# Kernel optimization log

Measured on AMD Instinct MI355X. Metric: run time of the kernel, lower is better.

## Reference

```python
import jax, jax.numpy as jnp
import numpy as np

B, T, IN, H = 512, 2048, 2, 128


def setup_inputs() -> dict:
    key = jax.random.key(0)
    ks = jax.random.split(key, 14)
    u = lambda k, shape: jax.random.uniform(k, shape, jnp.float32, -0.1, 0.1)
    return {
        "x": jax.random.normal(ks[0], (B, T, IN), jnp.float32),
        "mask": jnp.ones((B, T), jnp.float32),
        "emb_W": u(ks[1], (H, IN)), "emb_b": u(ks[2], (H,)),
        "enc_W": u(ks[3], (H, H)), "enc_b": u(ks[4], (H,)),
        "dec_input": u(ks[5], (H,)), "Vec": u(ks[6], (H,)),
        "Wq_W": u(ks[7], (H, H)), "Wq_b": u(ks[8], (H,)),
        "Wref_W": u(ks[9], (H, H)), "Wref_b": u(ks[10], (H,)),
        "fc1_W": u(ks[11], (H, H)), "fc2_W": u(ks[12], (2, H)),
    }


def reference(x, mask, emb_W, emb_b, enc_W, enc_b, dec_input, Vec,
              Wq_W, Wq_b, Wref_W, Wref_b, fc1_W, fc2_W):
    # Embedding: (B,T,IN) -> (B,T,H)
    x_embed = jnp.einsum("bti,hi->bth", x, emb_W) + emb_b
    # Encoder (stand-in for external Encoder class): per-token Linear + mask
    ref = (jnp.einsum("bti,hi->bth", x_embed, enc_W) + enc_b) * mask[:, :, None]

    def glimpse(query, ref):
        # query: (B,H); ref: (B,T,H)
        u1 = query @ Wq_W.T + Wq_b                                  # (B,H)
        # Conv1d kernel size 1 == pointwise linear over hidden dim
        u2 = jnp.einsum("bti,oi->bot", ref, Wref_W) + Wref_b[None, :, None]  # (B,H,T)
        u = jnp.einsum("h,bht->bt", Vec, jnp.tanh(u1[:, :, None] + u2))      # (B,T)
        a = jax.nn.softmax(u, axis=1)                               # (B,T)
        return jnp.einsum("bht,bt->bh", u2, a)                      # (B,H)

    query = jnp.broadcast_to(dec_input, (x.shape[0], dec_input.shape[0]))
    for _ in range(2):
        query = glimpse(query, ref)

    # final2FC: Linear(no bias) -> ReLU -> Linear(no bias); squeeze(-1) twice is a no-op (last dim=2)
    pred_l = jax.nn.relu(query @ fc1_W.T) @ fc2_W.T                 # (B,2)
    return pred_l
```

## Files before the change

### kernel.cpp

```cpp
#include <hip/hip_runtime.h>
#include <hip/hip_bf16.h>


#define Bsz 512
#define Tsz 2048
#define Hsz 128
#define THR 256
#define TOK 2
#define QB 4
static_assert(QB * THR * TOK == Tsz, "token tiling must cover each row exactly");

#define C2LOG2E 2.8853900817779268f
#define LOG2E   1.4426950408889634f

__device__ __forceinline__ float exp2fast(float x) { return __builtin_amdgcn_exp2f(x); }
__device__ __forceinline__ float rcpfast(float x)  { return __builtin_amdgcn_rcpf(x); }

__global__ __launch_bounds__(128) void kprep(
        const float* __restrict__ embW, const float* __restrict__ embB,
        const float* __restrict__ encW, const float* __restrict__ encB,
        const float* __restrict__ wrefW, const float* __restrict__ wrefB,
        const float* __restrict__ wqW, const float* __restrict__ wqB,
        const float* __restrict__ dec, const float* __restrict__ vec,
        float4* __restrict__ SCA, float4* __restrict__ UC, float* __restrict__ V2G) {
    __shared__ float m0[Hsz], m1[Hsz], cc[Hsz], dq[Hsz];
    int h = threadIdx.x;
    float a0 = 0.f, a1 = 0.f, ac = 0.f;
    for (int k = 0; k < Hsz; ++k) {
        float w = encW[h * Hsz + k];
        a0 = fmaf(w, embW[2 * k + 0], a0);
        a1 = fmaf(w, embW[2 * k + 1], a1);
        ac = fmaf(w, embB[k], ac);
    }
    m0[h] = a0; m1[h] = a1; cc[h] = ac + encB[h]; dq[h] = dec[h];
    __syncthreads();
    float p0 = 0.f, p1 = 0.f, pe = 0.f, uq = wqB[h];
    for (int k = 0; k < Hsz; ++k) {
        float w = wrefW[h * Hsz + k];
        p0 = fmaf(w, m0[k], p0);
        p1 = fmaf(w, m1[k], p1);
        pe = fmaf(w, cc[k], pe);
        uq = fmaf(wqW[h * Hsz + k], dq[k], uq);
    }
    float wb = wrefB[h];
    SCA[h] = make_float4(C2LOG2E * p0, C2LOG2E * p1, C2LOG2E * pe, C2LOG2E * (uq + wb));
    UC[h]  = make_float4(p0, p1, pe, wb);
    V2G[h] = 2.f * vec[h];
}

__global__ __launch_bounds__(THR) void kscore(
        const float* __restrict__ x, const float* __restrict__ mask,
        const float4* __restrict__ quadG, int bstride,
        const float* __restrict__ V2G,
        float4* __restrict__ statsOut) {
    __shared__ float4 quad[Hsz];
    __shared__ float v2s[Hsz];
    __shared__ float4 wr4[THR / 64];
    int blk = blockIdx.x, tid = threadIdx.x;
    int b = blk >> 2, qb = blk & 3;
    int wave = tid >> 6, lane = tid & 63;
    if (tid < Hsz) {
        quad[tid] = quadG[(size_t)b * bstride + tid];
        v2s[tid] = V2G[tid];
    }

    size_t tok0 = (size_t)b * Tsz + (size_t)qb * (THR * TOK);
    const float2* x2 = (const float2*)(x + tok0 * 2);
    const float* mrow = mask + tok0;
    float xm0[TOK], xm1[TOK], mk[TOK];
    #pragma unroll
    for (int j = 0; j < TOK; ++j) {
        float2 xv = x2[j * THR + tid];
        float m = mrow[j * THR + tid];
        mk[j] = m; xm0[j] = xv.x * m; xm1[j] = xv.y * m;
    }
    __syncthreads();

    float acc[TOK] = {0.f, 0.f};
    #pragma unroll 8
    for (int h = 0; h < Hsz; ++h) {
        float4 qd = quad[h];
        float vv = v2s[h];
        #pragma unroll
        for (int j = 0; j < TOK; ++j) {
            float a = fmaf(xm0[j], qd.x, fmaf(xm1[j], qd.y, fmaf(mk[j], qd.z, qd.w)));
            acc[j] = fmaf(vv, rcpfast(exp2fast(a) + 1.f), acc[j]);
        }
    }

    float Z = 0.f, Sm = 0.f, S0 = 0.f, S1 = 0.f;
    #pragma unroll
    for (int j = 0; j < TOK; ++j) {
        float e = exp2fast(-LOG2E * acc[j]);
        Z += e;
        Sm = fmaf(e, mk[j], Sm);
        S0 = fmaf(e, xm0[j], S0);
        S1 = fmaf(e, xm1[j], S1);
    }
    for (int off = 32; off; off >>= 1) {
        Z += __shfl_xor(Z, off); Sm += __shfl_xor(Sm, off);
        S0 += __shfl_xor(S0, off); S1 += __shfl_xor(S1, off);
    }
    if (lane == 0) wr4[wave] = make_float4(Z, Sm, S0, S1);
    __syncthreads();
    if (tid == 0) {
        float4 s = wr4[0];
        #pragma unroll
        for (int w = 1; w < THR / 64; ++w) {
            s.x += wr4[w].x; s.y += wr4[w].y; s.z += wr4[w].z; s.w += wr4[w].w;
        }
        statsOut[blk] = s;
    }
}

__global__ __launch_bounds__(128) void kmid(
        const float4* __restrict__ statsA, const float4* __restrict__ UC,
        const float4* __restrict__ SCA,
        const float* __restrict__ wqW, const float* __restrict__ wqB,
        float4* __restrict__ QB1) {
    __shared__ float q[Hsz];
    int b = blockIdx.x, tid = threadIdx.x;
    float Z = 0.f, Sm = 0.f, S0 = 0.f, S1 = 0.f;
    #pragma unroll
    for (int i = 0; i < QB; ++i) {
        float4 t = statsA[b * QB + i];
        Z += t.x; Sm += t.y; S0 += t.z; S1 += t.w;
    }
    float inv = 1.f / Z;
    float X0 = S0 * inv, X1 = S1 * inv, Cm = Sm * inv;
    float4 u4 = UC[tid];
    q[tid] = fmaf(X0, u4.x, fmaf(X1, u4.y, fmaf(Cm, u4.z, u4.w)));
    __syncthreads();
    float s = wqB[tid];
    const float* wr = wqW + (size_t)tid * Hsz;
    #pragma unroll 8
    for (int k = 0; k < Hsz; ++k) s = fmaf(wr[k], q[k], s);
    float4 sc = SCA[tid];
    QB1[b * Hsz + tid] = make_float4(sc.x, sc.y, sc.z, C2LOG2E * (s + u4.w));
}

__global__ __launch_bounds__(128) void kfin(
        const float4* __restrict__ statsB, const float4* __restrict__ UC,
        const float* __restrict__ fc1, const float* __restrict__ fc2,
        float* __restrict__ out) {
    __shared__ float q[Hsz], rr[Hsz];
    int b = blockIdx.x, tid = threadIdx.x;
    float Z = 0.f, Sm = 0.f, S0 = 0.f, S1 = 0.f;
    #pragma unroll
    for (int i = 0; i < QB; ++i) {
        float4 t = statsB[b * QB + i];
        Z += t.x; Sm += t.y; S0 += t.z; S1 += t.w;
    }
    float inv = 1.f / Z;
    float X0 = S0 * inv, X1 = S1 * inv, Cm = Sm * inv;
    float4 u4 = UC[tid];
    q[tid] = fmaf(X0, u4.x, fmaf(X1, u4.y, fmaf(Cm, u4.z, u4.w)));
    __syncthreads();
    float s = 0.f;
    const float* fr = fc1 + (size_t)tid * Hsz;
    #pragma unroll 8
    for (int k = 0; k < Hsz; ++k) s = fmaf(fr[k], q[k], s);
    rr[tid] = fmaxf(s, 0.f);
    __syncthreads();
    int o = tid >> 6, l = tid & 63;
    float s2 = fc2[o * Hsz + l] * rr[l] + fc2[o * Hsz + 64 + l] * rr[64 + l];
    for (int off = 32; off; off >>= 1) s2 += __shfl_xor(s2, off);
    if (l == 0) out[b * 2 + o] = s2;
}

extern "C" void kernel_launch(void* const* d_in, const int* in_sizes, int n_in,
                              void* d_out, int out_size, void* d_ws, size_t ws_size,
                              hipStream_t stream) {
    const float* x     = (const float*)d_in[0];
    const float* mask  = (const float*)d_in[1];
    const float* embW  = (const float*)d_in[2];
    const float* embB  = (const float*)d_in[3];
    const float* encW  = (const float*)d_in[4];
    const float* encB  = (const float*)d_in[5];
    const float* dec   = (const float*)d_in[6];
    const float* vec   = (const float*)d_in[7];
    const float* wqW   = (const float*)d_in[8];
    const float* wqB   = (const float*)d_in[9];
    const float* wrefW = (const float*)d_in[10];
    const float* wrefB = (const float*)d_in[11];
    const float* fc1   = (const float*)d_in[12];
    const float* fc2   = (const float*)d_in[13];

    float* ws = (float*)d_ws;
    float4* SCA    = (float4*)(ws + 0);
    float4* UC     = (float4*)(ws + 512);
    float*  V2G    = ws + 1024;
    float4* QB1    = (float4*)(ws + 1536);
    float4* statsA = (float4*)(ws + 263680);
    float4* statsB = (float4*)(ws + 271872);
    float* out = (float*)d_out;

    kprep<<<1, 128, 0, stream>>>(embW, embB, encW, encB, wrefW, wrefB, wqW, wqB,
                                 dec, vec, SCA, UC, V2G);
    kscore<<<Bsz * QB, THR, 0, stream>>>(x, mask, SCA, 0, V2G, statsA);
    kmid<<<Bsz, 128, 0, stream>>>(statsA, UC, SCA, wqW, wqB, QB1);
    kscore<<<Bsz * QB, THR, 0, stream>>>(x, mask, QB1, Hsz, V2G, statsB);
    kfin<<<Bsz, 128, 0, stream>>>(statsB, UC, fc1, fc2, out);
}
```

Measured before the change: 91.80 us.

## Split hidden dim across waves and factor query term out of exp

```diff
diff --git a/kernel.cpp b/kernel.cpp
--- a/kernel.cpp
+++ b/kernel.cpp
@@ -5,10 +5,15 @@
 #define Bsz 512
 #define Tsz 2048
 #define Hsz 128
-#define THR 256
-#define TOK 2
-#define QB 4
-static_assert(QB * THR * TOK == Tsz, "token tiling must cover each row exactly");
+#define TPB 1024
+#define WAVES 16
+#define HPW 8
+#define TTILE 256
+#define QB 8
+#define JT (TTILE / 64)
+static_assert(WAVES * HPW == Hsz, "h coverage");
+static_assert(QB * TTILE == Tsz, "token tiling must cover each row exactly");
+static_assert(WAVES * 64 == TPB, "wave count");
 
 #define C2LOG2E 2.8853900817779268f
 #define LOG2E   1.4426950408889634f
@@ -22,7 +27,7 @@
         const float* __restrict__ wrefW, const float* __restrict__ wrefB,
         const float* __restrict__ wqW, const float* __restrict__ wqB,
         const float* __restrict__ dec, const float* __restrict__ vec,
-        float4* __restrict__ SCA, float4* __restrict__ UC, float* __restrict__ V2G) {
+        float4* __restrict__ SCB, float* __restrict__ eD0, float4* __restrict__ UC) {
     __shared__ float m0[Hsz], m1[Hsz], cc[Hsz], dq[Hsz];
     int h = threadIdx.x;
     float a0 = 0.f, a1 = 0.f, ac = 0.f;
@@ -43,81 +48,91 @@
         uq = fmaf(wqW[h * Hsz + k], dq[k], uq);
     }
     float wb = wrefB[h];
-    SCA[h] = make_float4(C2LOG2E * p0, C2LOG2E * p1, C2LOG2E * pe, C2LOG2E * (uq + wb));
+    SCB[h] = make_float4(C2LOG2E * p0, C2LOG2E * p1, C2LOG2E * pe, 2.f * vec[h]);
+    float arg = C2LOG2E * (uq + wb);
+    eD0[h] = exp2fast(fminf(fmaxf(arg, -120.f), 120.f));
     UC[h]  = make_float4(p0, p1, pe, wb);
-    V2G[h] = 2.f * vec[h];
-}
-
-__global__ __launch_bounds__(THR) void kscore(
+}
+
+__global__ __launch_bounds__(TPB) void kscore(
         const float* __restrict__ x, const float* __restrict__ mask,
-        const float4* __restrict__ quadG, int bstride,
-        const float* __restrict__ V2G,
+        const float4* __restrict__ SCB,
+        const float* __restrict__ eDG, int bstride,
         float4* __restrict__ statsOut) {
-    __shared__ float4 quad[Hsz];
-    __shared__ float v2s[Hsz];
-    __shared__ float4 wr4[THR / 64];
+    __shared__ float pu[WAVES][TTILE];
+    __shared__ float4 wr4[4];
     int blk = blockIdx.x, tid = threadIdx.x;
-    int b = blk >> 2, qb = blk & 3;
-    int wave = tid >> 6, lane = tid & 63;
-    if (tid < Hsz) {
-        quad[tid] = quadG[(size_t)b * bstride + tid];
-        v2s[tid] = V2G[tid];
-    }
-
-    size_t tok0 = (size_t)b * Tsz + (size_t)qb * (THR * TOK);
-    const float2* x2 = (const float2*)(x + tok0 * 2);
+    int b = blk >> 3, qb = blk & 7;
+    int wv = __builtin_amdgcn_readfirstlane(tid >> 6);
+    int lane = tid & 63;
+
+    float cA[HPW], cB[HPW], cC[HPW], cV[HPW], cD[HPW];
+    {
+        const float4* cbase = SCB + wv * HPW;
+        const float* dbase = eDG + (size_t)b * bstride + wv * HPW;
+        #pragma unroll
+        for (int i = 0; i < HPW; ++i) {
+            float4 c = cbase[i];
+            cA[i] = c.x; cB[i] = c.y; cC[i] = c.z; cV[i] = c.w;
+            cD[i] = dbase[i];
+        }
+    }
+
+    size_t tok0 = (size_t)b * Tsz + (size_t)qb * TTILE;
+    const float2* x2 = (const float2*)x + tok0;
     const float* mrow = mask + tok0;
-    float xm0[TOK], xm1[TOK], mk[TOK];
+
     #pragma unroll
-    for (int j = 0; j < TOK; ++j) {
-        float2 xv = x2[j * THR + tid];
-        float m = mrow[j * THR + tid];
-        mk[j] = m; xm0[j] = xv.x * m; xm1[j] = xv.y * m;
-    }
-    __syncthreads();
-
-    float acc[TOK] = {0.f, 0.f};
-    #pragma unroll 8
-    for (int h = 0; h < Hsz; ++h) {
-        float4 qd = quad[h];
-        float vv = v2s[h];
+    for (int jt = 0; jt < JT; ++jt) {
+        int t = jt * 64 + lane;
+        float2 xv = x2[t];
+        float m = mrow[t];
+        float xm0 = xv.x * m, xm1 = xv.y * m;
+        float a0 = 0.f, a1 = 0.f;
         #pragma unroll
-        for (int j = 0; j < TOK; ++j) {
-            float a = fmaf(xm0[j], qd.x, fmaf(xm1[j], qd.y, fmaf(mk[j], qd.z, qd.w)));
-            acc[j] = fmaf(vv, rcpfast(exp2fast(a) + 1.f), acc[j]);
+        for (int i = 0; i < HPW; i += 2) {
+            float p  = fmaf(xm0, cA[i],   fmaf(xm1, cB[i],   m * cC[i]));
+            float d  = fmaf(exp2fast(p),  cD[i],   1.f);
+            a0 = fmaf(cV[i],   rcpfast(d),  a0);
+            float p2 = fmaf(xm0, cA[i+1], fmaf(xm1, cB[i+1], m * cC[i+1]));
+            float d2 = fmaf(exp2fast(p2), cD[i+1], 1.f);
+            a1 = fmaf(cV[i+1], rcpfast(d2), a1);
         }
-    }
+        pu[wv][t] = a0 + a1;
+    }
+    __syncthreads();
 
     float Z = 0.f, Sm = 0.f, S0 = 0.f, S1 = 0.f;
-    #pragma unroll
-    for (int j = 0; j < TOK; ++j) {
-        float e = exp2fast(-LOG2E * acc[j]);
-        Z += e;
-        Sm = fmaf(e, mk[j], Sm);
-        S0 = fmaf(e, xm0[j], S0);
-        S1 = fmaf(e, xm1[j], S1);
+    if (tid < TTILE) {
+        float s = 0.f;
+        #pragma unroll
+        for (int w = 0; w < WAVES; ++w) s += pu[w][tid];
+        float e = exp2fast(-LOG2E * s);
+        float2 xv = x2[tid];
+        float m = mrow[tid];
+        float em = e * m;
+        Z = e; Sm = em;
+        S0 = em * xv.x; S1 = em * xv.y;
     }
     for (int off = 32; off; off >>= 1) {
         Z += __shfl_xor(Z, off); Sm += __shfl_xor(Sm, off);
         S0 += __shfl_xor(S0, off); S1 += __shfl_xor(S1, off);
     }
-    if (lane == 0) wr4[wave] = make_float4(Z, Sm, S0, S1);
+    if (lane == 0 && wv < 4) wr4[wv] = make_float4(Z, Sm, S0, S1);
     __syncthreads();
     if (tid == 0) {
-        float4 s = wr4[0];
-        #pragma unroll
-        for (int w = 1; w < THR / 64; ++w) {
-            s.x += wr4[w].x; s.y += wr4[w].y; s.z += wr4[w].z; s.w += wr4[w].w;
-        }
-        statsOut[blk] = s;
+        float4 s0 = wr4[0], s1 = wr4[1], s2 = wr4[2], s3 = wr4[3];
+        statsOut[blk] = make_float4(s0.x + s1.x + s2.x + s3.x,
+                                    s0.y + s1.y + s2.y + s3.y,
+                                    s0.z + s1.z + s2.z + s3.z,
+                                    s0.w + s1.w + s2.w + s3.w);
     }
 }
 
 __global__ __launch_bounds__(128) void kmid(
         const float4* __restrict__ statsA, const float4* __restrict__ UC,
-        const float4* __restrict__ SCA,
         const float* __restrict__ wqW, const float* __restrict__ wqB,
-        float4* __restrict__ QB1) {
+        float* __restrict__ ED1) {
     __shared__ float q[Hsz];
     int b = blockIdx.x, tid = threadIdx.x;
     float Z = 0.f, Sm = 0.f, S0 = 0.f, S1 = 0.f;
@@ -135,8 +150,8 @@
     const float* wr = wqW + (size_t)tid * Hsz;
     #pragma unroll 8
     for (int k = 0; k < Hsz; ++k) s = fmaf(wr[k], q[k], s);
-    float4 sc = SCA[tid];
-    QB1[b * Hsz + tid] = make_float4(sc.x, sc.y, sc.z, C2LOG2E * (s + u4.w));
+    float arg = C2LOG2E * (s + u4.w);
+    ED1[b * Hsz + tid] = exp2fast(fminf(fmaxf(arg, -120.f), 120.f));
 }
 
 __global__ __launch_bounds__(128) void kfin(
@@ -187,18 +202,18 @@
     const float* fc2   = (const float*)d_in[13];
 
     float* ws = (float*)d_ws;
-    float4* SCA    = (float4*)(ws + 0);
+    float4* SCB    = (float4*)(ws + 0);
     float4* UC     = (float4*)(ws + 512);
-    float*  V2G    = ws + 1024;
-    float4* QB1    = (float4*)(ws + 1536);
-    float4* statsA = (float4*)(ws + 263680);
-    float4* statsB = (float4*)(ws + 271872);
+    float*  eD0    = ws + 1024;
+    float*  ED1    = ws + 1536;
+    float4* statsA = (float4*)(ws + 67072);
+    float4* statsB = (float4*)(ws + 83456);
     float* out = (float*)d_out;
 
     kprep<<<1, 128, 0, stream>>>(embW, embB, encW, encB, wrefW, wrefB, wqW, wqB,
-                                 dec, vec, SCA, UC, V2G);
-    kscore<<<Bsz * QB, THR, 0, stream>>>(x, mask, SCA, 0, V2G, statsA);
-    kmid<<<Bsz, 128, 0, stream>>>(statsA, UC, SCA, wqW, wqB, QB1);
-    kscore<<<Bsz * QB, THR, 0, stream>>>(x, mask, QB1, Hsz, V2G, statsB);
+                                 dec, vec, SCB, eD0, UC);
+    kscore<<<Bsz * QB, TPB, 0, stream>>>(x, mask, SCB, eD0, 0, statsA);
+    kmid<<<Bsz, 128, 0, stream>>>(statsA, UC, wqW, wqB, ED1);
+    kscore<<<Bsz * QB, TPB, 0, stream>>>(x, mask, SCB, ED1, Hsz, statsB);
     kfin<<<Bsz, 128, 0, stream>>>(statsB, UC, fc1, fc2, out);
 }
```

After: 104.6 us. 13.9% more time.
